# Kernel optimization log

Measured on AMD Instinct MI355X. Metric: run time of the kernel, lower is better.

The kernel has to match this reference:

```python
import jax, jax.numpy as jnp
import numpy as np

DIM = 512
HEADS = 8
HEAD_DIM = DIM // HEADS
WIN = 7
GC = DIM // 4
EPS = 1e-5


def dwconv1d(x, w, b):
    # x: (B, Cg, L), w: (Cg, 1, k) depthwise, b: (Cg,)
    k = w.shape[-1]
    out = jax.lax.conv_general_dilated(
        x, w, window_strides=(1,), padding=[(k // 2, k // 2)],
        dimension_numbers=("NCH", "OIH", "NCH"), feature_group_count=x.shape[1])
    return out + b[None, :, None]


def group_norm(x, groups, w, b):
    # x: (B, C, *spatial); normalize over (C//groups, *spatial) per group
    shp = x.shape
    xg = x.reshape(shp[0], groups, -1)
    mu = xg.mean(-1, keepdims=True)
    var = xg.var(-1, keepdims=True)
    xn = ((xg - mu) / jnp.sqrt(var + EPS)).reshape(shp)
    bshape = (1, shp[1]) + (1,) * (x.ndim - 2)
    return xn * w.reshape(bshape) + b.reshape(bshape)


def setup_inputs() -> dict:
    key = jax.random.key(0)
    ks = jax.random.split(key, 16)
    inp = {
        "x": jax.random.normal(ks[0], (32, DIM, 56, 56), dtype=jnp.float32),
        "w3": jax.random.normal(ks[1], (GC, 1, 3), dtype=jnp.float32) * 0.2,
        "b3": jax.random.normal(ks[2], (GC,), dtype=jnp.float32) * 0.02,
        "w5": jax.random.normal(ks[3], (GC, 1, 5), dtype=jnp.float32) * 0.2,
        "b5": jax.random.normal(ks[4], (GC,), dtype=jnp.float32) * 0.02,
        "w7": jax.random.normal(ks[5], (GC, 1, 7), dtype=jnp.float32) * 0.2,
        "b7": jax.random.normal(ks[6], (GC,), dtype=jnp.float32) * 0.02,
        "w9": jax.random.normal(ks[7], (GC, 1, 9), dtype=jnp.float32) * 0.2,
        "b9": jax.random.normal(ks[8], (GC,), dtype=jnp.float32) * 0.02,
        "gnh_w": jnp.ones((DIM,), jnp.float32),
        "gnh_b": jnp.zeros((DIM,), jnp.float32),
        "gnw_w": jnp.ones((DIM,), jnp.float32),
        "gnw_b": jnp.zeros((DIM,), jnp.float32),
        "gn_w": jnp.ones((DIM,), jnp.float32),
        "gn_b": jnp.zeros((DIM,), jnp.float32),
        "qw": jax.random.normal(ks[9], (DIM,), dtype=jnp.float32) * 0.2,
        "kw": jax.random.normal(ks[10], (DIM,), dtype=jnp.float32) * 0.2,
        "vw": jax.random.normal(ks[11], (DIM,), dtype=jnp.float32) * 0.2,
    }
    return inp


def reference(x, w3, b3, w5, b5, w7, b7, w9, b9,
              gnh_w, gnh_b, gnw_w, gnw_b, gn_w, gn_b, qw, kw, vw):
    B, C, H, W = x.shape
    ws = [(w3, b3), (w5, b5), (w7, b7), (w9, b9)]

    def multi_dwc(xp):  # xp: (B, C, L)
        parts = jnp.split(xp, 4, axis=1)
        return jnp.concatenate([dwconv1d(p, w, b) for p, (w, b) in zip(parts, ws)], axis=1)

    x_h = x.mean(axis=3)  # (B, C, H)
    x_w = x.mean(axis=2)  # (B, C, W)
    x_h_attn = jax.nn.sigmoid(group_norm(multi_dwc(x_h), 4, gnh_w, gnh_b))  # (B,C,H)
    x_w_attn = jax.nn.sigmoid(group_norm(multi_dwc(x_w), 4, gnw_w, gnw_b))  # (B,C,W)
    xg = x * x_h_attn[:, :, :, None] * x_w_attn[:, :, None, :]

    # avg-pool downsample by window_size
    hh, ww = H // WIN, W // WIN
    y = xg.reshape(B, C, hh, WIN, ww, WIN).mean(axis=(3, 5))  # (B,C,hh,ww)
    y = group_norm(y, 1, gn_w, gn_b)

    L = hh * ww
    q = (y * qw[None, :, None, None]).reshape(B, HEADS, HEAD_DIM, L)
    k = (y * kw[None, :, None, None]).reshape(B, HEADS, HEAD_DIM, L)
    v = (y * vw[None, :, None, None]).reshape(B, HEADS, HEAD_DIM, L)

    scaler = HEAD_DIM ** -0.5
    attn = jnp.einsum("bhdl,bhel->bhde", q, k) * scaler  # (B,H,d,d) channel attention
    attn = jax.nn.softmax(attn, axis=-1)
    out = jnp.einsum("bhde,bhel->bhdl", attn, v)  # (B,H,d,L)
    out = out.reshape(B, C, hh, ww)

    ca = jax.nn.sigmoid(out.mean(axis=(2, 3), keepdims=True))  # (B,C,1,1)
    return ca * xg
```

## Files before the change

kernel.cpp:

```cpp
#include <hip/hip_runtime.h>
#include <hip/hip_bf16.h>
#include <math.h>

#define B_     32
#define C_     512
#define HW_    56
#define PLANE  (HW_*HW_)
#define PLANE4 (PLANE/4)
#define GC_    128
#define WIN_   7
#define L2_    64
#define HEADS_ 8
#define HD_    64
#define EPS_   1e-5f

typedef float floatx4 __attribute__((ext_vector_type(4)));

__global__ __launch_bounds__(256) void k_means(const float* __restrict__ x,
                                               float* __restrict__ xh,
                                               float* __restrict__ xw) {
    const int bc = blockIdx.x;
    const int t  = threadIdx.x;
    __shared__ float lds[PLANE];
    __shared__ float rp[224];
    __shared__ float cp[224];

    const float4* p4 = (const float4*)(x + (size_t)bc * PLANE);
    for (int f = t; f < PLANE4; f += 256) {
        float4 v = p4[f];
        int base = f * 4;
        lds[base]   = v.x; lds[base+1] = v.y;
        lds[base+2] = v.z; lds[base+3] = v.w;
    }
    __syncthreads();

    if (t < 224) {
        int r = t >> 2, q = t & 3;
        float s = 0.f;
        int base = r * HW_ + q * 14;
        #pragma unroll
        for (int i = 0; i < 14; i++) s += lds[base + i];
        rp[t] = s;
        float s2 = 0.f;
        int cbase = q * 14 * HW_ + r;
        #pragma unroll
        for (int i = 0; i < 14; i++) s2 += lds[cbase + i * HW_];
        cp[t] = s2;
    }
    __syncthreads();

    if (t < HW_) {
        float rs = rp[4*t] + rp[4*t+1] + rp[4*t+2] + rp[4*t+3];
        xh[(size_t)bc * HW_ + t] = rs * (1.0f / HW_);
        float cs = cp[4*t] + cp[4*t+1] + cp[4*t+2] + cp[4*t+3];
        xw[(size_t)bc * HW_ + t] = cs * (1.0f / HW_);
    }
}

__global__ __launch_bounds__(256) void k_conv_gn_sig(
    const float* __restrict__ xh, const float* __restrict__ xw,
    const float* __restrict__ w3, const float* __restrict__ b3,
    const float* __restrict__ w5, const float* __restrict__ b5,
    const float* __restrict__ w7, const float* __restrict__ b7,
    const float* __restrict__ w9, const float* __restrict__ b9,
    const float* __restrict__ gnh_w, const float* __restrict__ gnh_b,
    const float* __restrict__ gnw_w, const float* __restrict__ gnw_b,
    float* __restrict__ ah, float* __restrict__ aw) {

    const int blk = blockIdx.x;
    const int b = blk >> 3;
    const int which = (blk & 7) >> 2;
    const int g = blk & 3;
    const int t = threadIdx.x;

    const float* in  = (which ? xw : xh) + ((size_t)(b * C_ + g * GC_)) * HW_;
    float*       out = (which ? aw : ah) + ((size_t)(b * C_ + g * GC_)) * HW_;
    const float* gw  = (which ? gnw_w : gnh_w) + g * GC_;
    const float* gb  = (which ? gnw_b : gnh_b) + g * GC_;

    const float* wsel; const float* bsel; int ks;
    switch (g) {
        case 0:  wsel = w3; bsel = b3; ks = 3; break;
        case 1:  wsel = w5; bsel = b5; ks = 5; break;
        case 2:  wsel = w7; bsel = b7; ks = 7; break;
        default: wsel = w9; bsel = b9; ks = 9; break;
    }

    __shared__ float lin[GC_ * HW_];
    __shared__ float wl[GC_ * 9];
    __shared__ float bl[GC_];
    __shared__ float red[10];

    for (int i = t; i < GC_ * HW_; i += 256) lin[i] = in[i];
    const int nw = GC_ * ks;
    for (int i = t; i < nw; i += 256) wl[i] = wsel[i];
    if (t < GC_) bl[t] = bsel[t];
    __syncthreads();

    const int k2 = ks >> 1;
    float acc[28];
    float s = 0.f, s2 = 0.f;
    #pragma unroll
    for (int k = 0; k < 28; k++) {
        int idx = t + k * 256;
        int c = idx / HW_, l = idx % HW_;
        float a = bl[c];
        for (int tt = 0; tt < ks; tt++) {
            int pos = l + tt - k2;
            if (pos >= 0 && pos < HW_) a += wl[c * ks + tt] * lin[c * HW_ + pos];
        }
        acc[k] = a;
        s += a; s2 += a * a;
    }

    #pragma unroll
    for (int o = 32; o > 0; o >>= 1) { s += __shfl_down(s, o); s2 += __shfl_down(s2, o); }
    int lane = t & 63, wid = t >> 6;
    if (lane == 0) { red[wid] = s; red[4 + wid] = s2; }
    __syncthreads();
    if (t == 0) {
        float S  = red[0] + red[1] + red[2] + red[3];
        float S2 = red[4] + red[5] + red[6] + red[7];
        float mean = S * (1.0f / (GC_ * HW_));
        float var  = S2 * (1.0f / (GC_ * HW_)) - mean * mean;
        red[8] = mean;
        red[9] = rsqrtf(var + EPS_);
    }
    __syncthreads();
    const float mean = red[8], rstd = red[9];

    #pragma unroll
    for (int k = 0; k < 28; k++) {
        int idx = t + k * 256;
        int c = idx / HW_;
        float v = (acc[k] - mean) * rstd * gw[c] + gb[c];
        out[idx] = 1.0f / (1.0f + expf(-v));
    }
}

__global__ __launch_bounds__(256) void k_pool(const float* __restrict__ x,
                                              const float* __restrict__ ah,
                                              const float* __restrict__ aw,
                                              float* __restrict__ y) {
    const int bc = blockIdx.x;
    const int t  = threadIdx.x;
    __shared__ float lds[PLANE];
    __shared__ float a_h[HW_];
    __shared__ float a_w[HW_];

    if (t < HW_) {
        a_h[t] = ah[(size_t)bc * HW_ + t];
        a_w[t] = aw[(size_t)bc * HW_ + t];
    }
    __syncthreads();

    const float4* p4 = (const float4*)(x + (size_t)bc * PLANE);
    for (int f = t; f < PLANE4; f += 256) {
        float4 v = p4[f];
        int h = f / 14, jb = (f % 14) * 4;
        float m = a_h[h];
        int base = h * HW_ + jb;
        lds[base]   = v.x * m * a_w[jb];
        lds[base+1] = v.y * m * a_w[jb+1];
        lds[base+2] = v.z * m * a_w[jb+2];
        lds[base+3] = v.w * m * a_w[jb+3];
    }
    __syncthreads();

    if (t < L2_) {
        int hh = t >> 3, ww = t & 7;
        float s = 0.f;
        #pragma unroll
        for (int i = 0; i < WIN_; i++)
            #pragma unroll
            for (int j = 0; j < WIN_; j++)
                s += lds[(WIN_*hh + i) * HW_ + WIN_*ww + j];
        y[(size_t)bc * L2_ + t] = s * (1.0f / (WIN_*WIN_));
    }
}

__global__ __launch_bounds__(256) void k_attn(const float* __restrict__ y,
                                              const float* __restrict__ gn_w,
                                              const float* __restrict__ gn_b,
                                              const float* __restrict__ qw,
                                              const float* __restrict__ kw,
                                              const float* __restrict__ vw,
                                              float* __restrict__ ca) {
    const int blk = blockIdx.x;
    const int b = blk >> 3, h = blk & 7;
    const int t = threadIdx.x;

    __shared__ float qs[HD_][68];
    __shared__ float ks_[HD_][68];
    __shared__ float att[HD_][68];
    __shared__ float vbar[HD_];
    __shared__ float red[10];

    {
        const float4* yb4 = (const float4*)(y + (size_t)b * (C_ * L2_));
        float s = 0.f, s2 = 0.f;
        for (int i = t; i < (C_ * L2_ / 4); i += 256) {
            float4 v = yb4[i];
            s  += v.x + v.y + v.z + v.w;
            s2 += v.x*v.x + v.y*v.y + v.z*v.z + v.w*v.w;
        }
        #pragma unroll
        for (int o = 32; o > 0; o >>= 1) { s += __shfl_down(s, o); s2 += __shfl_down(s2, o); }
        int lane = t & 63, wid = t >> 6;
        if (lane == 0) { red[wid] = s; red[4 + wid] = s2; }
        __syncthreads();
        if (t == 0) {
            float S  = red[0] + red[1] + red[2] + red[3];
            float S2 = red[4] + red[5] + red[6] + red[7];
            float mean = S * (1.0f / (C_ * L2_));
            float var  = S2 * (1.0f / (C_ * L2_)) - mean * mean;
            red[8] = mean;
            red[9] = rsqrtf(var + EPS_);
        }
        __syncthreads();
    }
    const float mu = red[8], rstd = red[9];

    const float4* yp4 = (const float4*)(y + ((size_t)(b * C_ + h * HD_)) * L2_);

    for (int f = t; f < 1024; f += 256) {
        int d = f >> 4, lb = (f & 15) << 2;
        int ch = h * HD_ + d;
        float gsc = gn_w[ch] * rstd;
        float gof = gn_b[ch] - mu * gsc;
        float qg = qw[ch], kg = kw[ch];
        float4 v = yp4[f];
        float y0 = v.x * gsc + gof, y1 = v.y * gsc + gof;
        float y2 = v.z * gsc + gof, y3 = v.w * gsc + gof;
        qs[d][lb]   = y0 * qg; qs[d][lb+1] = y1 * qg;
        qs[d][lb+2] = y2 * qg; qs[d][lb+3] = y3 * qg;
        ks_[d][lb]   = y0 * kg; ks_[d][lb+1] = y1 * kg;
        ks_[d][lb+2] = y2 * kg; ks_[d][lb+3] = y3 * kg;
        att[d][lb]   = y0; att[d][lb+1] = y1;
        att[d][lb+2] = y2; att[d][lb+3] = y3;
    }
    __syncthreads();

    if (t < HD_) {
        int ch = h * HD_ + t;
        float s = 0.f;
        #pragma unroll
        for (int l = 0; l < L2_; l++) s += att[t][l];
        vbar[t] = s * (1.0f / L2_) * vw[ch];
    }
    __syncthreads();

    const int d = t >> 2, eb = t & 3;
    float acc[16];
    #pragma unroll
    for (int i = 0; i < 16; i++) acc[i] = 0.f;
    #pragma unroll 4
    for (int lb = 0; lb < 16; lb++) {
        float4 qv = *(const float4*)&qs[d][lb * 4];
        #pragma unroll
        for (int i = 0; i < 16; i++) {
            float4 kv = *(const float4*)&ks_[eb + 4*i][lb * 4];
            acc[i] += qv.x * kv.x + qv.y * kv.y + qv.z * kv.z + qv.w * kv.w;
        }
    }
    __syncthreads();
    #pragma unroll
    for (int i = 0; i < 16; i++) att[d][eb + 4*i] = acc[i] * 0.125f;
    __syncthreads();

    {
        float m = -1e30f;
        #pragma unroll
        for (int i = 0; i < 16; i++) m = fmaxf(m, att[d][eb * 16 + i]);
        m = fmaxf(m, __shfl_xor(m, 1));
        m = fmaxf(m, __shfl_xor(m, 2));
        float s1 = 0.f, s2 = 0.f;
        #pragma unroll
        for (int i = 0; i < 16; i++) {
            int e = eb * 16 + i;
            float p = expf(att[d][e] - m);
            s1 += p;
            s2 += p * vbar[e];
        }
        s1 += __shfl_xor(s1, 1); s2 += __shfl_xor(s2, 1);
        s1 += __shfl_xor(s1, 2); s2 += __shfl_xor(s2, 2);
        if (eb == 0) {
            float o = s2 / s1;
            ca[(size_t)b * C_ + h * HD_ + d] = 1.0f / (1.0f + expf(-o));
        }
    }
}

__global__ __launch_bounds__(256) void k_out(const float* __restrict__ x,
                                             const float* __restrict__ ah,
                                             const float* __restrict__ aw,
                                             const float* __restrict__ ca,
                                             float* __restrict__ out) {
    const unsigned total4 = (unsigned)B_ * C_ * PLANE4;
    const unsigned stride = gridDim.x * blockDim.x;
    const floatx4* px = (const floatx4*)x;
    floatx4*       po = (floatx4*)out;

    for (unsigned i = blockIdx.x * blockDim.x + threadIdx.x; i < total4; i += stride) {
        unsigned bc = i / PLANE4;
        unsigned r  = i - bc * PLANE4;
        unsigned hh = r / 14;
        unsigned jb = (r - hh * 14) * 4;

        floatx4 v  = px[i];
        floatx4 w4 = *(const floatx4*)&aw[bc * HW_ + jb];
        float   m  = ca[bc] * ah[bc * HW_ + hh];
        v.x *= m * w4.x;
        v.y *= m * w4.y;
        v.z *= m * w4.z;
        v.w *= m * w4.w;
        __builtin_nontemporal_store(v, &po[i]);
    }
}

extern "C" void kernel_launch(void* const* d_in, const int* in_sizes, int n_in,
                              void* d_out, int out_size, void* d_ws, size_t ws_size,
                              hipStream_t stream) {
    const float* x     = (const float*)d_in[0];
    const float* w3    = (const float*)d_in[1];
    const float* b3    = (const float*)d_in[2];
    const float* w5    = (const float*)d_in[3];
    const float* b5    = (const float*)d_in[4];
    const float* w7    = (const float*)d_in[5];
    const float* b7    = (const float*)d_in[6];
    const float* w9    = (const float*)d_in[7];
    const float* b9    = (const float*)d_in[8];
    const float* gnh_w = (const float*)d_in[9];
    const float* gnh_b = (const float*)d_in[10];
    const float* gnw_w = (const float*)d_in[11];
    const float* gnw_b = (const float*)d_in[12];
    const float* gn_w  = (const float*)d_in[13];
    const float* gn_b  = (const float*)d_in[14];
    const float* qw    = (const float*)d_in[15];
    const float* kw    = (const float*)d_in[16];
    const float* vw    = (const float*)d_in[17];

    float* ws = (float*)d_ws;
    const size_t N_BC56 = (size_t)B_ * C_ * HW_;
    float* xh    = ws;
    float* xw    = xh + N_BC56;
    float* ah    = xw + N_BC56;
    float* aw    = ah + N_BC56;
    float* yy    = aw + N_BC56;
    float* ca    = yy + (size_t)B_ * C_ * L2_;

    const int nbc = B_ * C_;

    k_means<<<nbc, 256, 0, stream>>>(x, xh, xw);
    k_conv_gn_sig<<<B_ * 8, 256, 0, stream>>>(xh, xw, w3, b3, w5, b5, w7, b7, w9, b9,
                                              gnh_w, gnh_b, gnw_w, gnw_b, ah, aw);
    k_pool<<<nbc, 256, 0, stream>>>(x, ah, aw, yy);
    k_attn<<<B_ * HEADS_, 256, 0, stream>>>(yy, gn_w, gn_b, qw, kw, vw, ca);
    k_out<<<2048, 256, 0, stream>>>(x, ah, aw, ca, (float*)d_out);
}
```

Measured before the change: 173.5 us.

## Fuse all stages into one cooperative persistent kernel with grid syncs

Replaces the five separate kernel launches with a single cooperative kernel that runs the means, conv+groupnorm+sigmoid, pooling, channel attention and output scaling stages separated by grid.sync, using a grid capped at 1024 blocks. It also folds the h/w attention gates into the pooling sum instead of scaling every element, and applies the q/k per-channel weights after the dot product so only one normalized tile is kept in LDS. Stages that use only 256 blocks leave most of the grid idle at each barrier, and grid-wide syncs add cost. The old multi-kernel path remains as a fallback if the cooperative launch fails.

Result: slower. 516.1 us (+197.5%).

```diff
diff --git a/kernel.cpp b/kernel.cpp
--- a/kernel.cpp
+++ b/kernel.cpp
@@ -1,20 +1,294 @@
 #include <hip/hip_runtime.h>
-#include <hip/hip_bf16.h>
+#include <hip/hip_cooperative_groups.h>
 #include <math.h>
+
+namespace cg = cooperative_groups;
 
 #define B_     32
 #define C_     512
 #define HW_    56
-#define PLANE  (HW_*HW_)
-#define PLANE4 (PLANE/4)
+#define PLANE  3136
+#define PLANE4 784
 #define GC_    128
-#define WIN_   7
 #define L2_    64
-#define HEADS_ 8
 #define HD_    64
 #define EPS_   1e-5f
+#define NBC    (B_*C_)
 
 typedef float floatx4 __attribute__((ext_vector_type(4)));
+
+#define SMEM_F 4432
+
+__global__ __launch_bounds__(256, 4) void k_fused(
+    const float* __restrict__ x,
+    const float* __restrict__ w3, const float* __restrict__ b3,
+    const float* __restrict__ w5, const float* __restrict__ b5,
+    const float* __restrict__ w7, const float* __restrict__ b7,
+    const float* __restrict__ w9, const float* __restrict__ b9,
+    const float* __restrict__ gnh_w, const float* __restrict__ gnh_b,
+    const float* __restrict__ gnw_w, const float* __restrict__ gnw_b,
+    const float* __restrict__ gn_w, const float* __restrict__ gn_b,
+    const float* __restrict__ qw, const float* __restrict__ kw,
+    const float* __restrict__ vw,
+    float* __restrict__ xh, float* __restrict__ xw_,
+    float* __restrict__ ah, float* __restrict__ aw,
+    float* __restrict__ yy, float* __restrict__ ca,
+    float* __restrict__ out)
+{
+    cg::grid_group grid = cg::this_grid();
+    const int t    = threadIdx.x;
+    const int blk  = blockIdx.x;
+    const int nblk = gridDim.x;
+    __shared__ float smem[SMEM_F];
+
+    for (int bc = blk; bc < NBC; bc += nblk) {
+        const floatx4* p4 = (const floatx4*)(x + (size_t)bc * PLANE);
+        for (int f = t; f < PLANE4; f += 256) {
+            floatx4 v = p4[f];
+            int base = f * 4;
+            smem[base]   = v.x; smem[base+1] = v.y;
+            smem[base+2] = v.z; smem[base+3] = v.w;
+        }
+        __syncthreads();
+        if (t < 224) {
+            int r = t >> 2, q = t & 3;
+            float s = 0.f;
+            int base = r * HW_ + q * 14;
+            #pragma unroll
+            for (int i = 0; i < 14; i++) s += smem[base + i];
+            smem[3136 + t] = s;
+            float s2 = 0.f;
+            int cb = q * 14 * HW_ + r;
+            #pragma unroll
+            for (int i = 0; i < 14; i++) s2 += smem[cb + i * HW_];
+            smem[3360 + t] = s2;
+        }
+        __syncthreads();
+        if (t < HW_) {
+            float rs = smem[3136+4*t] + smem[3136+4*t+1] + smem[3136+4*t+2] + smem[3136+4*t+3];
+            xh[(size_t)bc * HW_ + t] = rs * (1.0f / HW_);
+            float cs = smem[3360+4*t] + smem[3360+4*t+1] + smem[3360+4*t+2] + smem[3360+4*t+3];
+            xw_[(size_t)bc * HW_ + t] = cs * (1.0f / HW_);
+        }
+        __syncthreads();
+    }
+    grid.sync();
+
+    if (blk < 256) {
+        const int b     = blk >> 3;
+        const int which = (blk & 7) >> 2;
+        const int g     = blk & 3;
+
+        const float* in  = (which ? xw_ : xh) + ((size_t)(b * C_ + g * GC_)) * HW_;
+        float*       o   = (which ? aw  : ah) + ((size_t)(b * C_ + g * GC_)) * HW_;
+        const float* gw  = (which ? gnw_w : gnh_w) + g * GC_;
+        const float* gb  = (which ? gnw_b : gnh_b) + g * GC_;
+
+        const float* wsel; const float* bsel; int ks;
+        switch (g) {
+            case 0:  wsel = w3; bsel = b3; ks = 3; break;
+            case 1:  wsel = w5; bsel = b5; ks = 5; break;
+            case 2:  wsel = w7; bsel = b7; ks = 7; break;
+            default: wsel = w9; bsel = b9; ks = 9; break;
+        }
+        float* wl  = smem;
+        float* bl  = smem + 1152;
+        float* red = smem + 4416;
+
+        const int nw = GC_ * ks;
+        for (int i = t; i < nw; i += 256) wl[i] = wsel[i];
+        if (t < GC_) bl[t] = bsel[t];
+        __syncthreads();
+
+        const int k2 = ks >> 1;
+        float s = 0.f, s2 = 0.f;
+        #pragma unroll
+        for (int k = 0; k < 28; k++) {
+            int idx = t + k * 256;
+            int c = idx / HW_, l = idx - c * HW_;
+            float a = bl[c];
+            for (int tt = 0; tt < ks; tt++) {
+                int pos = l + tt - k2;
+                if (pos >= 0 && pos < HW_) a += wl[c * ks + tt] * in[c * HW_ + pos];
+            }
+            s += a; s2 += a * a;
+        }
+        #pragma unroll
+        for (int off = 32; off > 0; off >>= 1) { s += __shfl_down(s, off); s2 += __shfl_down(s2, off); }
+        int lane = t & 63, wid = t >> 6;
+        if (lane == 0) { red[wid] = s; red[4 + wid] = s2; }
+        __syncthreads();
+        if (t == 0) {
+            float S  = red[0] + red[1] + red[2] + red[3];
+            float S2 = red[4] + red[5] + red[6] + red[7];
+            float mean = S * (1.0f / (GC_ * HW_));
+            float var  = S2 * (1.0f / (GC_ * HW_)) - mean * mean;
+            red[8] = mean;
+            red[9] = rsqrtf(var + EPS_);
+        }
+        __syncthreads();
+        const float mean = red[8], rstd = red[9];
+
+        #pragma unroll
+        for (int k = 0; k < 28; k++) {
+            int idx = t + k * 256;
+            int c = idx / HW_, l = idx - c * HW_;
+            float a = bl[c];
+            for (int tt = 0; tt < ks; tt++) {
+                int pos = l + tt - k2;
+                if (pos >= 0 && pos < HW_) a += wl[c * ks + tt] * in[c * HW_ + pos];
+            }
+            float v = (a - mean) * rstd * gw[c] + gb[c];
+            o[idx] = 1.0f / (1.0f + expf(-v));
+        }
+    }
+    grid.sync();
+
+    for (int bc = blk; bc < NBC; bc += nblk) {
+        if (t < HW_) {
+            smem[3136 + t] = ah[(size_t)bc * HW_ + t];
+            smem[3192 + t] = aw[(size_t)bc * HW_ + t];
+        }
+        const floatx4* p4 = (const floatx4*)(x + (size_t)bc * PLANE);
+        for (int f = t; f < PLANE4; f += 256) {
+            floatx4 v = p4[f];
+            int base = f * 4;
+            smem[base]   = v.x; smem[base+1] = v.y;
+            smem[base+2] = v.z; smem[base+3] = v.w;
+        }
+        __syncthreads();
+        if (t < L2_) {
+            int hh = t >> 3, ww = t & 7;
+            float s = 0.f;
+            #pragma unroll
+            for (int i = 0; i < 7; i++) {
+                float rsum = 0.f;
+                int rbase = (7*hh + i) * HW_ + 7*ww;
+                #pragma unroll
+                for (int j = 0; j < 7; j++) rsum += smem[rbase + j] * smem[3192 + 7*ww + j];
+                s += rsum * smem[3136 + 7*hh + i];
+            }
+            yy[(size_t)bc * L2_ + t] = s * (1.0f / 49.0f);
+        }
+        __syncthreads();
+    }
+    grid.sync();
+
+    if (blk < 256) {
+        const int b = blk >> 3, h = blk & 7;
+        float* yn   = smem;
+        float* vbar = smem + 4352;
+        float* red  = smem + 4416;
+
+        {
+            const floatx4* yb4 = (const floatx4*)(yy + (size_t)b * (C_ * L2_));
+            float s = 0.f, s2 = 0.f;
+            for (int i = t; i < (C_ * L2_ / 4); i += 256) {
+                floatx4 v = yb4[i];
+                s  += v.x + v.y + v.z + v.w;
+                s2 += v.x*v.x + v.y*v.y + v.z*v.z + v.w*v.w;
+            }
+            #pragma unroll
+            for (int off = 32; off > 0; off >>= 1) { s += __shfl_down(s, off); s2 += __shfl_down(s2, off); }
+            int lane = t & 63, wid = t >> 6;
+            if (lane == 0) { red[wid] = s; red[4 + wid] = s2; }
+            __syncthreads();
+            if (t == 0) {
+                float S  = red[0] + red[1] + red[2] + red[3];
+                float S2 = red[4] + red[5] + red[6] + red[7];
+                float mean = S * (1.0f / (C_ * L2_));
+                float var  = S2 * (1.0f / (C_ * L2_)) - mean * mean;
+                red[8] = mean;
+                red[9] = rsqrtf(var + EPS_);
+            }
+            __syncthreads();
+        }
+        const float mu = red[8], rstd = red[9];
+
+        const floatx4* yp4 = (const floatx4*)(yy + ((size_t)(b * C_ + h * HD_)) * L2_);
+        for (int f = t; f < 1024; f += 256) {
+            int d = f >> 4, lb = (f & 15) << 2;
+            int ch = h * HD_ + d;
+            float gsc = gn_w[ch] * rstd;
+            float gof = gn_b[ch] - mu * gsc;
+            floatx4 v = yp4[f];
+            yn[d*68 + lb]   = v.x * gsc + gof;
+            yn[d*68 + lb+1] = v.y * gsc + gof;
+            yn[d*68 + lb+2] = v.z * gsc + gof;
+            yn[d*68 + lb+3] = v.w * gsc + gof;
+        }
+        __syncthreads();
+
+        if (t < HD_) {
+            int ch = h * HD_ + t;
+            float s = 0.f;
+            #pragma unroll
+            for (int l = 0; l < L2_; l++) s += yn[t*68 + l];
+            vbar[t] = s * (1.0f / L2_) * vw[ch];
+        }
+        __syncthreads();
+
+        const int d = t >> 2, eb = t & 3;
+        const int ch0 = h * HD_;
+        float acc[16];
+        #pragma unroll
+        for (int i = 0; i < 16; i++) acc[i] = 0.f;
+        #pragma unroll 4
+        for (int lb = 0; lb < 16; lb++) {
+            floatx4 qv = *(const floatx4*)&yn[d*68 + lb*4];
+            #pragma unroll
+            for (int i = 0; i < 16; i++) {
+                floatx4 kv = *(const floatx4*)&yn[(eb + 4*i)*68 + lb*4];
+                acc[i] += qv.x*kv.x + qv.y*kv.y + qv.z*kv.z + qv.w*kv.w;
+            }
+        }
+        const float qg = qw[ch0 + d] * 0.125f;
+        float m = -1e30f;
+        #pragma unroll
+        for (int i = 0; i < 16; i++) {
+            acc[i] *= qg * kw[ch0 + eb + 4*i];
+            m = fmaxf(m, acc[i]);
+        }
+        m = fmaxf(m, __shfl_xor(m, 1));
+        m = fmaxf(m, __shfl_xor(m, 2));
+        float s1 = 0.f, s2 = 0.f;
+        #pragma unroll
+        for (int i = 0; i < 16; i++) {
+            float p = expf(acc[i] - m);
+            s1 += p;
+            s2 += p * vbar[eb + 4*i];
+        }
+        s1 += __shfl_xor(s1, 1); s2 += __shfl_xor(s2, 1);
+        s1 += __shfl_xor(s1, 2); s2 += __shfl_xor(s2, 2);
+        if (eb == 0) {
+            float o = s2 / s1;
+            ca[(size_t)b * C_ + ch0 + d] = 1.0f / (1.0f + expf(-o));
+        }
+    }
+    grid.sync();
+
+    {
+        const unsigned total4 = (unsigned)B_ * C_ * PLANE4;
+        const unsigned stride = nblk * 256;
+        const floatx4* px = (const floatx4*)x;
+        floatx4*       po = (floatx4*)out;
+        for (unsigned i = blk * 256 + t; i < total4; i += stride) {
+            unsigned bc = i / PLANE4;
+            unsigned r  = i - bc * PLANE4;
+            unsigned hh = r / 14;
+            unsigned jb = (r - hh * 14) * 4;
+
+            floatx4 v  = px[i];
+            floatx4 w4 = *(const floatx4*)&aw[bc * HW_ + jb];
+            float   mm = ca[bc] * ah[bc * HW_ + hh];
+            v.x *= mm * w4.x;
+            v.y *= mm * w4.y;
+            v.z *= mm * w4.z;
+            v.w *= mm * w4.w;
+            __builtin_nontemporal_store(v, &po[i]);
+        }
+    }
+}
 
 __global__ __launch_bounds__(256) void k_means(const float* __restrict__ x,
                                                float* __restrict__ xh,
@@ -25,15 +299,14 @@
     __shared__ float rp[224];
     __shared__ float cp[224];
 
-    const float4* p4 = (const float4*)(x + (size_t)bc * PLANE);
+    const floatx4* p4 = (const floatx4*)(x + (size_t)bc * PLANE);
     for (int f = t; f < PLANE4; f += 256) {
-        float4 v = p4[f];
+        floatx4 v = p4[f];
         int base = f * 4;
         lds[base]   = v.x; lds[base+1] = v.y;
         lds[base+2] = v.z; lds[base+3] = v.w;
     }
     __syncthreads();
-
     if (t < 224) {
         int r = t >> 2, q = t & 3;
         float s = 0.f;
@@ -48,7 +321,6 @@
         cp[t] = s2;
     }
     __syncthreads();
-
     if (t < HW_) {
         float rs = rp[4*t] + rp[4*t+1] + rp[4*t+2] + rp[4*t+3];
         xh[(size_t)bc * HW_ + t] = rs * (1.0f / HW_);
@@ -103,7 +375,7 @@
     #pragma unroll
     for (int k = 0; k < 28; k++) {
         int idx = t + k * 256;
-        int c = idx / HW_, l = idx % HW_;
+        int c = idx / HW_, l = idx - c * HW_;
         float a = bl[c];
         for (int tt = 0; tt < ks; tt++) {
             int pos = l + tt - k2;
@@ -112,7 +384,6 @@
         acc[k] = a;
         s += a; s2 += a * a;
     }
-
     #pragma unroll
     for (int o = 32; o > 0; o >>= 1) { s += __shfl_down(s, o); s2 += __shfl_down(s2, o); }
     int lane = t & 63, wid = t >> 6;
@@ -152,30 +423,26 @@
         a_h[t] = ah[(size_t)bc * HW_ + t];
         a_w[t] = aw[(size_t)bc * HW_ + t];
     }
-    __syncthreads();
-
-    const float4* p4 = (const float4*)(x + (size_t)bc * PLANE);
+    const floatx4* p4 = (const floatx4*)(x + (size_t)bc * PLANE);
     for (int f = t; f < PLANE4; f += 256) {
-        float4 v = p4[f];
-        int h = f / 14, jb = (f % 14) * 4;
-        float m = a_h[h];
-        int base = h * HW_ + jb;
-        lds[base]   = v.x * m * a_w[jb];
-        lds[base+1] = v.y * m * a_w[jb+1];
-        lds[base+2] = v.z * m * a_w[jb+2];
-        lds[base+3] = v.w * m * a_w[jb+3];
-    }
-    __syncthreads();
-
+        floatx4 v = p4[f];
+        int base = f * 4;
+        lds[base]   = v.x; lds[base+1] = v.y;
+        lds[base+2] = v.z; lds[base+3] = v.w;
+    }
+    __syncthreads();
     if (t < L2_) {
         int hh = t >> 3, ww = t & 7;
         float s = 0.f;
         #pragma unroll
-        for (int i = 0; i < WIN_; i++)
+        for (int i = 0; i < 7; i++) {
+            float rsum = 0.f;
+            int rbase = (7*hh + i) * HW_ + 7*ww;
             #pragma unroll
-            for (int j = 0; j < WIN_; j++)
-                s += lds[(WIN_*hh + i) * HW_ + WIN_*ww + j];
-        y[(size_t)bc * L2_ + t] = s * (1.0f / (WIN_*WIN_));
+            for (int j = 0; j < 7; j++) rsum += lds[rbase + j] * a_w[7*ww + j];
+            s += rsum * a_h[7*hh + i];
+        }
+        y[(size_t)bc * L2_ + t] = s * (1.0f / 49.0f);
     }
 }
 
@@ -190,22 +457,20 @@
     const int b = blk >> 3, h = blk & 7;
     const int t = threadIdx.x;
 
-    __shared__ float qs[HD_][68];
-    __shared__ float ks_[HD_][68];
-    __shared__ float att[HD_][68];
+    __shared__ float yn[HD_ * 68];
     __shared__ float vbar[HD_];
     __shared__ float red[10];
 
     {
-        const float4* yb4 = (const float4*)(y + (size_t)b * (C_ * L2_));
+        const floatx4* yb4 = (const floatx4*)(y + (size_t)b * (C_ * L2_));
         float s = 0.f, s2 = 0.f;
         for (int i = t; i < (C_ * L2_ / 4); i += 256) {
-            float4 v = yb4[i];
+            floatx4 v = yb4[i];
             s  += v.x + v.y + v.z + v.w;
             s2 += v.x*v.x + v.y*v.y + v.z*v.z + v.w*v.w;
         }
         #pragma unroll
-        for (int o = 32; o > 0; o >>= 1) { s += __shfl_down(s, o); s2 += __shfl_down(s2, o); }
+        for (int off = 32; off > 0; off >>= 1) { s += __shfl_down(s, off); s2 += __shfl_down(s2, off); }
         int lane = t & 63, wid = t >> 6;
         if (lane == 0) { red[wid] = s; red[4 + wid] = s2; }
         __syncthreads();
@@ -221,23 +486,17 @@
     }
     const float mu = red[8], rstd = red[9];
 
-    const float4* yp4 = (const float4*)(y + ((size_t)(b * C_ + h * HD_)) * L2_);
-
+    const floatx4* yp4 = (const floatx4*)(y + ((size_t)(b * C_ + h * HD_)) * L2_);
     for (int f = t; f < 1024; f += 256) {
         int d = f >> 4, lb = (f & 15) << 2;
         int ch = h * HD_ + d;
         float gsc = gn_w[ch] * rstd;
         float gof = gn_b[ch] - mu * gsc;
-        float qg = qw[ch], kg = kw[ch];
-        float4 v = yp4[f];
-        float y0 = v.x * gsc + gof, y1 = v.y * gsc + gof;
-        float y2 = v.z * gsc + gof, y3 = v.w * gsc + gof;
-        qs[d][lb]   = y0 * qg; qs[d][lb+1] = y1 * qg;
-        qs[d][lb+2] = y2 * qg; qs[d][lb+3] = y3 * qg;
-        ks_[d][lb]   = y0 * kg; ks_[d][lb+1] = y1 * kg;
-        ks_[d][lb+2] = y2 * kg; ks_[d][lb+3] = y3 * kg;
-        att[d][lb]   = y0; att[d][lb+1] = y1;
-        att[d][lb+2] = y2; att[d][lb+3] = y3;
+        floatx4 v = yp4[f];
+        yn[d*68 + lb]   = v.x * gsc + gof;
+        yn[d*68 + lb+1] = v.y * gsc + gof;
+        yn[d*68 + lb+2] = v.z * gsc + gof;
+        yn[d*68 + lb+3] = v.w * gsc + gof;
     }
     __syncthreads();
 
@@ -245,49 +504,46 @@
         int ch = h * HD_ + t;
         float s = 0.f;
         #pragma unroll
-        for (int l = 0; l < L2_; l++) s += att[t][l];
+        for (int l = 0; l < L2_; l++) s += yn[t*68 + l];
         vbar[t] = s * (1.0f / L2_) * vw[ch];
     }
     __syncthreads();
 
     const int d = t >> 2, eb = t & 3;
+    const int ch0 = h * HD_;
     float acc[16];
     #pragma unroll
     for (int i = 0; i < 16; i++) acc[i] = 0.f;
     #pragma unroll 4
     for (int lb = 0; lb < 16; lb++) {
-        float4 qv = *(const float4*)&qs[d][lb * 4];
+        floatx4 qv = *(const floatx4*)&yn[d*68 + lb*4];
         #pragma unroll
         for (int i = 0; i < 16; i++) {
-            float4 kv = *(const float4*)&ks_[eb + 4*i][lb * 4];
-            acc[i] += qv.x * kv.x + qv.y * kv.y + qv.z * kv.z + qv.w * kv.w;
-        }
-    }
-    __syncthreads();
+            floatx4 kv = *(const floatx4*)&yn[(eb + 4*i)*68 + lb*4];
+            acc[i] += qv.x*kv.x + qv.y*kv.y + qv.z*kv.z + qv.w*kv.w;
+        }
+    }
+    const float qg = qw[ch0 + d] * 0.125f;
+    float m = -1e30f;
     #pragma unroll
-    for (int i = 0; i < 16; i++) att[d][eb + 4*i] = acc[i] * 0.125f;
-    __syncthreads();
-
-    {
-        float m = -1e30f;
-        #pragma unroll
-        for (int i = 0; i < 16; i++) m = fmaxf(m, att[d][eb * 16 + i]);
-        m = fmaxf(m, __shfl_xor(m, 1));
-        m = fmaxf(m, __shfl_xor(m, 2));
-        float s1 = 0.f, s2 = 0.f;
-        #pragma unroll
-        for (int i = 0; i < 16; i++) {
-            int e = eb * 16 + i;
-            float p = expf(att[d][e] - m);
-            s1 += p;
-            s2 += p * vbar[e];
-        }
-        s1 += __shfl_xor(s1, 1); s2 += __shfl_xor(s2, 1);
-        s1 += __shfl_xor(s1, 2); s2 += __shfl_xor(s2, 2);
-        if (eb == 0) {
-            float o = s2 / s1;
-            ca[(size_t)b * C_ + h * HD_ + d] = 1.0f / (1.0f + expf(-o));
-        }
+    for (int i = 0; i < 16; i++) {
+        acc[i] *= qg * kw[ch0 + eb + 4*i];
+        m = fmaxf(m, acc[i]);
+    }
+    m = fmaxf(m, __shfl_xor(m, 1));
+    m = fmaxf(m, __shfl_xor(m, 2));
+    float s1 = 0.f, s2 = 0.f;
+    #pragma unroll
+    for (int i = 0; i < 16; i++) {
+        float p = expf(acc[i] - m);
+        s1 += p;
+        s2 += p * vbar[eb + 4*i];
+    }
+    s1 += __shfl_xor(s1, 1); s2 += __shfl_xor(s2, 1);
+    s1 += __shfl_xor(s1, 2); s2 += __shfl_xor(s2, 2);
+    if (eb == 0) {
+        float o = s2 / s1;
+        ca[(size_t)b * C_ + ch0 + d] = 1.0f / (1.0f + expf(-o));
     }
 }
 
@@ -342,19 +598,48 @@
 
     float* ws = (float*)d_ws;
     const size_t N_BC56 = (size_t)B_ * C_ * HW_;
-    float* xh    = ws;
-    float* xw    = xh + N_BC56;
-    float* ah    = xw + N_BC56;
-    float* aw    = ah + N_BC56;
-    float* yy    = aw + N_BC56;
-    float* ca    = yy + (size_t)B_ * C_ * L2_;
-
-    const int nbc = B_ * C_;
-
-    k_means<<<nbc, 256, 0, stream>>>(x, xh, xw);
-    k_conv_gn_sig<<<B_ * 8, 256, 0, stream>>>(xh, xw, w3, b3, w5, b5, w7, b7, w9, b9,
-                                              gnh_w, gnh_b, gnw_w, gnw_b, ah, aw);
-    k_pool<<<nbc, 256, 0, stream>>>(x, ah, aw, yy);
-    k_attn<<<B_ * HEADS_, 256, 0, stream>>>(yy, gn_w, gn_b, qw, kw, vw, ca);
-    k_out<<<2048, 256, 0, stream>>>(x, ah, aw, ca, (float*)d_out);
+    float* xh  = ws;
+    float* xw_ = xh + N_BC56;
+    float* ah  = xw_ + N_BC56;
+    float* aw  = ah + N_BC56;
+    float* yy  = aw + N_BC56;
+    float* ca  = yy + (size_t)B_ * C_ * L2_;
+    float* out = (float*)d_out;
+
+    int maxPerCU = 0;
+    hipError_t qerr = hipOccupancyMaxActiveBlocksPerMultiprocessor(
+        &maxPerCU, (const void*)k_fused, 256, 0);
+    int numCU = 0;
+    hipError_t derr = hipDeviceGetAttribute(&numCU, hipDeviceAttributeMultiprocessorCount, 0);
+    int grid = 0;
+    if (qerr == hipSuccess && derr == hipSuccess && maxPerCU > 0 && numCU > 0) {
+        long cap = (long)maxPerCU * numCU;
+        grid = (int)(cap < 1024 ? cap : 1024);
+    }
+
+    hipError_t lerr = hipErrorUnknown;
+    if (grid >= 256) {
+        void* args[] = {
+            (void*)&x,
+            (void*)&w3, (void*)&b3, (void*)&w5, (void*)&b5,
+            (void*)&w7, (void*)&b7, (void*)&w9, (void*)&b9,
+            (void*)&gnh_w, (void*)&gnh_b, (void*)&gnw_w, (void*)&gnw_b,
+            (void*)&gn_w, (void*)&gn_b,
+            (void*)&qw, (void*)&kw, (void*)&vw,
+            (void*)&xh, (void*)&xw_, (void*)&ah, (void*)&aw,
+            (void*)&yy, (void*)&ca, (void*)&out,
+        };
+        lerr = hipLaunchCooperativeKernel((void*)k_fused, dim3(grid), dim3(256),
+                                          args, 0, stream);
+    }
+
+    if (lerr != hipSuccess) {
+        const int nbc = B_ * C_;
+        k_means<<<nbc, 256, 0, stream>>>(x, xh, xw_);
+        k_conv_gn_sig<<<B_ * 8, 256, 0, stream>>>(xh, xw_, w3, b3, w5, b5, w7, b7, w9, b9,
+                                                  gnh_w, gnh_b, gnw_w, gnw_b, ah, aw);
+        k_pool<<<nbc, 256, 0, stream>>>(x, ah, aw, yy);
+        k_attn<<<B_ * 8, 256, 0, stream>>>(yy, gn_w, gn_b, qw, kw, vw, ca);
+        k_out<<<2048, 256, 0, stream>>>(x, ah, aw, ca, out);
+    }
 }
```

## Fuse groupnorm stats into pool via atomics and factor q/k scales out of attention

Applied to the files above, without the earlier changes.

The pool kernel now loads x unscaled into LDS and applies the h/w attention weights factorized inside the 7x7 window sum. It also reduces per-batch sum and sum-of-squares and adds them with atomics into a stats buffer that k_means zeroes. The attention kernel reads those stats instead of re-reducing the whole batch slice of y in every block. It keeps a single normalized y tile in LDS, applying the per-channel q/k scales to the dot products afterwards, which drops two LDS arrays and a sync round. The costs are atomic contention and float atomics making the result order-dependent and nondeterministic.

Result: slower. 349.1 us (+101.3%).

```diff
diff --git a/kernel.cpp b/kernel.cpp
--- a/kernel.cpp
+++ b/kernel.cpp
@@ -1,16 +1,13 @@
 #include <hip/hip_runtime.h>
-#include <hip/hip_bf16.h>
 #include <math.h>
 
 #define B_     32
 #define C_     512
 #define HW_    56
-#define PLANE  (HW_*HW_)
-#define PLANE4 (PLANE/4)
+#define PLANE  3136
+#define PLANE4 784
 #define GC_    128
-#define WIN_   7
 #define L2_    64
-#define HEADS_ 8
 #define HD_    64
 #define EPS_   1e-5f
 
@@ -18,22 +15,24 @@
 
 __global__ __launch_bounds__(256) void k_means(const float* __restrict__ x,
                                                float* __restrict__ xh,
-                                               float* __restrict__ xw) {
+                                               float* __restrict__ xw,
+                                               float* __restrict__ stats) {
     const int bc = blockIdx.x;
     const int t  = threadIdx.x;
     __shared__ float lds[PLANE];
     __shared__ float rp[224];
     __shared__ float cp[224];
 
-    const float4* p4 = (const float4*)(x + (size_t)bc * PLANE);
+    if (bc == 0 && t < 2 * B_) stats[t] = 0.f;
+
+    const floatx4* p4 = (const floatx4*)(x + (size_t)bc * PLANE);
     for (int f = t; f < PLANE4; f += 256) {
-        float4 v = p4[f];
+        floatx4 v = p4[f];
         int base = f * 4;
         lds[base]   = v.x; lds[base+1] = v.y;
         lds[base+2] = v.z; lds[base+3] = v.w;
     }
     __syncthreads();
-
     if (t < 224) {
         int r = t >> 2, q = t & 3;
         float s = 0.f;
@@ -48,7 +47,6 @@
         cp[t] = s2;
     }
     __syncthreads();
-
     if (t < HW_) {
         float rs = rp[4*t] + rp[4*t+1] + rp[4*t+2] + rp[4*t+3];
         xh[(size_t)bc * HW_ + t] = rs * (1.0f / HW_);
@@ -86,12 +84,16 @@
         default: wsel = w9; bsel = b9; ks = 9; break;
     }
 
-    __shared__ float lin[GC_ * HW_];
+    __shared__ __align__(16) float lin[GC_ * HW_];
     __shared__ float wl[GC_ * 9];
     __shared__ float bl[GC_];
     __shared__ float red[10];
 
-    for (int i = t; i < GC_ * HW_; i += 256) lin[i] = in[i];
+    {
+        const floatx4* in4 = (const floatx4*)in;
+        floatx4* lin4 = (floatx4*)lin;
+        for (int i = t; i < GC_ * HW_ / 4; i += 256) lin4[i] = in4[i];
+    }
     const int nw = GC_ * ks;
     for (int i = t; i < nw; i += 256) wl[i] = wsel[i];
     if (t < GC_) bl[t] = bsel[t];
@@ -103,7 +105,7 @@
     #pragma unroll
     for (int k = 0; k < 28; k++) {
         int idx = t + k * 256;
-        int c = idx / HW_, l = idx % HW_;
+        int c = idx / HW_, l = idx - c * HW_;
         float a = bl[c];
         for (int tt = 0; tt < ks; tt++) {
             int pos = l + tt - k2;
@@ -112,7 +114,6 @@
         acc[k] = a;
         s += a; s2 += a * a;
     }
-
     #pragma unroll
     for (int o = 32; o > 0; o >>= 1) { s += __shfl_down(s, o); s2 += __shfl_down(s2, o); }
     int lane = t & 63, wid = t >> 6;
@@ -141,7 +142,8 @@
 __global__ __launch_bounds__(256) void k_pool(const float* __restrict__ x,
                                               const float* __restrict__ ah,
                                               const float* __restrict__ aw,
-                                              float* __restrict__ y) {
+                                              float* __restrict__ y,
+                                              float* __restrict__ stats) {
     const int bc = blockIdx.x;
     const int t  = threadIdx.x;
     __shared__ float lds[PLANE];
@@ -152,34 +154,43 @@
         a_h[t] = ah[(size_t)bc * HW_ + t];
         a_w[t] = aw[(size_t)bc * HW_ + t];
     }
-    __syncthreads();
-
-    const float4* p4 = (const float4*)(x + (size_t)bc * PLANE);
+    const floatx4* p4 = (const floatx4*)(x + (size_t)bc * PLANE);
     for (int f = t; f < PLANE4; f += 256) {
-        float4 v = p4[f];
-        int h = f / 14, jb = (f % 14) * 4;
-        float m = a_h[h];
-        int base = h * HW_ + jb;
-        lds[base]   = v.x * m * a_w[jb];
-        lds[base+1] = v.y * m * a_w[jb+1];
-        lds[base+2] = v.z * m * a_w[jb+2];
-        lds[base+3] = v.w * m * a_w[jb+3];
-    }
-    __syncthreads();
-
+        floatx4 v = p4[f];
+        int base = f * 4;
+        lds[base]   = v.x; lds[base+1] = v.y;
+        lds[base+2] = v.z; lds[base+3] = v.w;
+    }
+    __syncthreads();
     if (t < L2_) {
         int hh = t >> 3, ww = t & 7;
         float s = 0.f;
         #pragma unroll
-        for (int i = 0; i < WIN_; i++)
+        for (int i = 0; i < 7; i++) {
+            float rsum = 0.f;
+            int rbase = (7*hh + i) * HW_ + 7*ww;
             #pragma unroll
-            for (int j = 0; j < WIN_; j++)
-                s += lds[(WIN_*hh + i) * HW_ + WIN_*ww + j];
-        y[(size_t)bc * L2_ + t] = s * (1.0f / (WIN_*WIN_));
+            for (int j = 0; j < 7; j++) rsum += lds[rbase + j] * a_w[7*ww + j];
+            s += rsum * a_h[7*hh + i];
+        }
+        float ps = s * (1.0f / 49.0f);
+        y[(size_t)bc * L2_ + t] = ps;
+        float a = ps, a2 = ps * ps;
+        #pragma unroll
+        for (int off = 32; off > 0; off >>= 1) {
+            a  += __shfl_down(a, off);
+            a2 += __shfl_down(a2, off);
+        }
+        if (t == 0) {
+            int b = bc >> 9;
+            atomicAdd(&stats[b], a);
+            atomicAdd(&stats[B_ + b], a2);
+        }
     }
 }
 
 __global__ __launch_bounds__(256) void k_attn(const float* __restrict__ y,
+                                              const float* __restrict__ stats,
                                               const float* __restrict__ gn_w,
                                               const float* __restrict__ gn_b,
                                               const float* __restrict__ qw,
@@ -190,54 +201,26 @@
     const int b = blk >> 3, h = blk & 7;
     const int t = threadIdx.x;
 
-    __shared__ float qs[HD_][68];
-    __shared__ float ks_[HD_][68];
-    __shared__ float att[HD_][68];
+    __shared__ float yn[HD_ * 68];
     __shared__ float vbar[HD_];
-    __shared__ float red[10];
-
-    {
-        const float4* yb4 = (const float4*)(y + (size_t)b * (C_ * L2_));
-        float s = 0.f, s2 = 0.f;
-        for (int i = t; i < (C_ * L2_ / 4); i += 256) {
-            float4 v = yb4[i];
-            s  += v.x + v.y + v.z + v.w;
-            s2 += v.x*v.x + v.y*v.y + v.z*v.z + v.w*v.w;
-        }
-        #pragma unroll
-        for (int o = 32; o > 0; o >>= 1) { s += __shfl_down(s, o); s2 += __shfl_down(s2, o); }
-        int lane = t & 63, wid = t >> 6;
-        if (lane == 0) { red[wid] = s; red[4 + wid] = s2; }
-        __syncthreads();
-        if (t == 0) {
-            float S  = red[0] + red[1] + red[2] + red[3];
-            float S2 = red[4] + red[5] + red[6] + red[7];
-            float mean = S * (1.0f / (C_ * L2_));
-            float var  = S2 * (1.0f / (C_ * L2_)) - mean * mean;
-            red[8] = mean;
-            red[9] = rsqrtf(var + EPS_);
-        }
-        __syncthreads();
-    }
-    const float mu = red[8], rstd = red[9];
-
-    const float4* yp4 = (const float4*)(y + ((size_t)(b * C_ + h * HD_)) * L2_);
-
+
+    const float S  = stats[b];
+    const float S2 = stats[B_ + b];
+    const float mu   = S * (1.0f / (C_ * L2_));
+    const float var  = S2 * (1.0f / (C_ * L2_)) - mu * mu;
+    const float rstd = rsqrtf(var + EPS_);
+
+    const floatx4* yp4 = (const floatx4*)(y + ((size_t)(b * C_ + h * HD_)) * L2_);
     for (int f = t; f < 1024; f += 256) {
         int d = f >> 4, lb = (f & 15) << 2;
         int ch = h * HD_ + d;
         float gsc = gn_w[ch] * rstd;
         float gof = gn_b[ch] - mu * gsc;
-        float qg = qw[ch], kg = kw[ch];
-        float4 v = yp4[f];
-        float y0 = v.x * gsc + gof, y1 = v.y * gsc + gof;
-        float y2 = v.z * gsc + gof, y3 = v.w * gsc + gof;
-        qs[d][lb]   = y0 * qg; qs[d][lb+1] = y1 * qg;
-        qs[d][lb+2] = y2 * qg; qs[d][lb+3] = y3 * qg;
-        ks_[d][lb]   = y0 * kg; ks_[d][lb+1] = y1 * kg;
-        ks_[d][lb+2] = y2 * kg; ks_[d][lb+3] = y3 * kg;
-        att[d][lb]   = y0; att[d][lb+1] = y1;
-        att[d][lb+2] = y2; att[d][lb+3] = y3;
+        floatx4 v = yp4[f];
+        yn[d*68 + lb]   = v.x * gsc + gof;
+        yn[d*68 + lb+1] = v.y * gsc + gof;
+        yn[d*68 + lb+2] = v.z * gsc + gof;
+        yn[d*68 + lb+3] = v.w * gsc + gof;
     }
     __syncthreads();
 
@@ -245,49 +228,46 @@
         int ch = h * HD_ + t;
         float s = 0.f;
         #pragma unroll
-        for (int l = 0; l < L2_; l++) s += att[t][l];
+        for (int l = 0; l < L2_; l++) s += yn[t*68 + l];
         vbar[t] = s * (1.0f / L2_) * vw[ch];
     }
     __syncthreads();
 
     const int d = t >> 2, eb = t & 3;
+    const int ch0 = h * HD_;
     float acc[16];
     #pragma unroll
     for (int i = 0; i < 16; i++) acc[i] = 0.f;
     #pragma unroll 4
     for (int lb = 0; lb < 16; lb++) {
-        float4 qv = *(const float4*)&qs[d][lb * 4];
+        floatx4 qv = *(const floatx4*)&yn[d*68 + lb*4];
         #pragma unroll
         for (int i = 0; i < 16; i++) {
-            float4 kv = *(const float4*)&ks_[eb + 4*i][lb * 4];
-            acc[i] += qv.x * kv.x + qv.y * kv.y + qv.z * kv.z + qv.w * kv.w;
-        }
-    }
-    __syncthreads();
-    #pragma unroll
-    for (int i = 0; i < 16; i++) att[d][eb + 4*i] = acc[i] * 0.125f;
-    __syncthreads();
-
-    {
-        float m = -1e30f;
-        #pragma unroll
-        for (int i = 0; i < 16; i++) m = fmaxf(m, att[d][eb * 16 + i]);
-        m = fmaxf(m, __shfl_xor(m, 1));
-        m = fmaxf(m, __shfl_xor(m, 2));
-        float s1 = 0.f, s2 = 0.f;
-        #pragma unroll
-        for (int i = 0; i < 16; i++) {
-            int e = eb * 16 + i;
-            float p = expf(att[d][e] - m);
-            s1 += p;
-            s2 += p * vbar[e];
-        }
-        s1 += __shfl_xor(s1, 1); s2 += __shfl_xor(s2, 1);
-        s1 += __shfl_xor(s1, 2); s2 += __shfl_xor(s2, 2);
-        if (eb == 0) {
-            float o = s2 / s1;
-            ca[(size_t)b * C_ + h * HD_ + d] = 1.0f / (1.0f + expf(-o));
-        }
+            floatx4 kv = *(const floatx4*)&yn[(eb + 4*i)*68 + lb*4];
+            acc[i] += qv.x*kv.x + qv.y*kv.y + qv.z*kv.z + qv.w*kv.w;
+        }
+    }
+    const float qg = qw[ch0 + d] * 0.125f;
+    float m = -1e30f;
+    #pragma unroll
+    for (int i = 0; i < 16; i++) {
+        acc[i] *= qg * kw[ch0 + eb + 4*i];
+        m = fmaxf(m, acc[i]);
+    }
+    m = fmaxf(m, __shfl_xor(m, 1));
+    m = fmaxf(m, __shfl_xor(m, 2));
+    float s1 = 0.f, s2 = 0.f;
+    #pragma unroll
+    for (int i = 0; i < 16; i++) {
+        float p = expf(acc[i] - m);
+        s1 += p;
+        s2 += p * vbar[eb + 4*i];
+    }
+    s1 += __shfl_xor(s1, 1); s2 += __shfl_xor(s2, 1);
+    s1 += __shfl_xor(s1, 2); s2 += __shfl_xor(s2, 2);
+    if (eb == 0) {
+        float o = s2 / s1;
+        ca[(size_t)b * C_ + ch0 + d] = 1.0f / (1.0f + expf(-o));
     }
 }
 
@@ -343,18 +323,19 @@
     float* ws = (float*)d_ws;
     const size_t N_BC56 = (size_t)B_ * C_ * HW_;
     float* xh    = ws;
-    float* xw    = xh + N_BC56;
-    float* ah    = xw + N_BC56;
+    float* xw_   = xh + N_BC56;
+    float* ah    = xw_ + N_BC56;
     float* aw    = ah + N_BC56;
     float* yy    = aw + N_BC56;
-    float* ca    = yy + (size_t)B_ * C_ * L2_;
+    float* stats = yy + (size_t)B_ * C_ * L2_;
+    float* ca    = stats + 2 * B_;
 
     const int nbc = B_ * C_;
 
-    k_means<<<nbc, 256, 0, stream>>>(x, xh, xw);
-    k_conv_gn_sig<<<B_ * 8, 256, 0, stream>>>(xh, xw, w3, b3, w5, b5, w7, b7, w9, b9,
+    k_means<<<nbc, 256, 0, stream>>>(x, xh, xw_, stats);
+    k_conv_gn_sig<<<B_ * 8, 256, 0, stream>>>(xh, xw_, w3, b3, w5, b5, w7, b7, w9, b9,
                                               gnh_w, gnh_b, gnw_w, gnw_b, ah, aw);
-    k_pool<<<nbc, 256, 0, stream>>>(x, ah, aw, yy);
-    k_attn<<<B_ * HEADS_, 256, 0, stream>>>(yy, gn_w, gn_b, qw, kw, vw, ca);
+    k_pool<<<nbc, 256, 0, stream>>>(x, ah, aw, yy, stats);
+    k_attn<<<B_ * 8, 256, 0, stream>>>(yy, stats, gn_w, gn_b, qw, kw, vw, ca);
     k_out<<<2048, 256, 0, stream>>>(x, ah, aw, ca, (float*)d_out);
 }
```
